# Kernel tuning notes

Measured on AMD Instinct MI355X. Metric: run time of the kernel, lower is better.

## Reference

```python
import jax, jax.numpy as jnp
import numpy as np


def setup_inputs() -> dict:
    key = jax.random.key(0)
    kq, kk, kv = jax.random.split(key, 3)
    S, D = 8192, 128
    return {
        "Q": jax.random.normal(kq, (S, D), dtype=jnp.float32),
        "K": jax.random.normal(kk, (S, D), dtype=jnp.float32),
        "V": jax.random.normal(kv, (S, D), dtype=jnp.float32),
    }


def reference(Q, K, V):
    d_k = Q.shape[-1]
    scale = 1.0 / jnp.sqrt(jnp.asarray(d_k, Q.dtype))
    scores = (Q @ K.T) * scale          # [S, S]
    attn = jax.nn.softmax(scores, axis=-1)
    return attn @ V                     # [S, Dv]
```

## Files before the change

kernel.cpp:

```cpp
#include <hip/hip_runtime.h>
#include <hip/hip_bf16.h>
#include <hip/hip_fp16.h>
#include <math.h>

typedef __attribute__((ext_vector_type(8))) short short8;
typedef __attribute__((ext_vector_type(16))) float f32x16;
typedef __attribute__((ext_vector_type(4))) unsigned short ushort4v;
typedef __attribute__((ext_vector_type(4))) unsigned int uint4v;

#define S 8192
#define D 128
#define QBLK 128
#define KVB 32

__device__ __forceinline__ unsigned short f2bf(float f) {
    unsigned int x = __float_as_uint(f);
    unsigned int r = x + 0x7fffu + ((x >> 16) & 1u);
    return (unsigned short)(r >> 16);
}

__device__ __forceinline__ unsigned int cvtpk(float a, float b) {
    unsigned int r;
    asm("v_cvt_pk_bf16_f32 %0, %1, %2" : "=v"(r) : "v"(a), "v"(b));
    return r;
}

__device__ __forceinline__ float fexp2(float x) { return __builtin_amdgcn_exp2f(x); }

__device__ __forceinline__ void gl_lds16(const unsigned short* g, unsigned short* l) {
    __builtin_amdgcn_global_load_lds(
        (const __attribute__((address_space(1))) unsigned int*)g,
        (__attribute__((address_space(3))) unsigned int*)l, 16, 0, 0);
}

__device__ __forceinline__ void plswap(unsigned int& a, unsigned int& b, int hi) {
#if __has_builtin(__builtin_amdgcn_permlane32_swap)
    auto r = __builtin_amdgcn_permlane32_swap((int)a, (int)b, false, false);
    a = (unsigned int)r[0];
    b = (unsigned int)r[1];
#else
    unsigned int xa = (unsigned int)__shfl_xor((int)a, 32, 64);
    unsigned int xb = (unsigned int)__shfl_xor((int)b, 32, 64);
    unsigned int na = hi ? xb : a;
    unsigned int nb = hi ? b : xa;
    a = na; b = nb;
#endif
}

union W4 { unsigned int u[4]; short8 v; };

__global__ __launch_bounds__(256) void prep_kv(const float* __restrict__ K,
                                               const float* __restrict__ V,
                                               unsigned short* __restrict__ Kb,
                                               unsigned short* __restrict__ Vt) {
    __shared__ unsigned short T[64][72];
    const float scale = 0.12751743022854459f;
    int s0 = blockIdx.x * 64, d0 = blockIdx.y * 64;
    int tr = threadIdx.x >> 4, tc = (threadIdx.x & 15) * 4;
#pragma unroll
    for (int p = 0; p < 4; ++p) {
        int r = p * 16 + tr;
        float4 kf = *reinterpret_cast<const float4*>(K + (size_t)(s0 + r) * D + d0 + tc);
        ushort4v ko = { f2bf(kf.x * scale), f2bf(kf.y * scale),
                        f2bf(kf.z * scale), f2bf(kf.w * scale) };
        *reinterpret_cast<ushort4v*>(Kb + (size_t)(s0 + r) * D + d0 + tc) = ko;
        float4 v = *reinterpret_cast<const float4*>(V + (size_t)(s0 + r) * D + d0 + tc);
        ushort4v vo = { f2bf(v.x), f2bf(v.y), f2bf(v.z), f2bf(v.w) };
        *reinterpret_cast<ushort4v*>(&T[r][tc]) = vo;
    }
    __syncthreads();
#pragma unroll
    for (int p = 0; p < 4; ++p) {
        int dr = p * 16 + tr;
        ushort4v o = { T[tc + 0][dr], T[tc + 1][dr], T[tc + 2][dr], T[tc + 3][dr] };
        *reinterpret_cast<ushort4v*>(Vt + (size_t)(d0 + dr) * S + s0 + tc) = o;
    }
}

#define QKOP(acc, kc) (acc) = __builtin_amdgcn_mfma_f32_32x32x16_bf16(              \
    *reinterpret_cast<const short8*>(                                               \
        &Kl[(size_t)c31 * 128 + (((2 * (kc) + hi) ^ (c31 & 15)) * 8)]),             \
    qf[kc], (acc), 0, 0, 0)

#define PVOP(oo, pp, dt, off) (oo) = __builtin_amdgcn_mfma_f32_32x32x16_bf16(       \
    (pp).v,                                                                          \
    *reinterpret_cast<const short8*>(                                               \
        &Vl[((dt) * 32 + c31) * 32 + ((((off) + hi) ^ sw) * 8)]),                    \
    (oo), 0, 0, 0)

#define SMEX(PD0, PD1)                                                               \
    {                                                                                \
        float e[16];                                                                 \
        _Pragma("unroll")                                                            \
        for (int i = 0; i < 16; ++i) e[i] = fexp2(sa[i] + sb[i]);                    \
        float t0 = (e[0] + e[1]) + (e[2] + e[3]);                                    \
        float t1 = (e[4] + e[5]) + (e[6] + e[7]);                                    \
        float t2 = (e[8] + e[9]) + (e[10] + e[11]);                                  \
        float t3 = (e[12] + e[13]) + (e[14] + e[15]);                                \
        l_r += (t0 + t1) + (t2 + t3);                                                \
        unsigned int wd[8];                                                          \
        _Pragma("unroll")                                                            \
        for (int u = 0; u < 8; ++u) wd[u] = cvtpk(e[2 * u], e[2 * u + 1]);           \
        plswap(wd[0], wd[2], hi); plswap(wd[1], wd[3], hi);                          \
        plswap(wd[4], wd[6], hi); plswap(wd[5], wd[7], hi);                          \
        PD0.u[0] = wd[0]; PD0.u[1] = wd[1]; PD0.u[2] = wd[2]; PD0.u[3] = wd[3];      \
        PD1.u[0] = wd[4]; PD1.u[1] = wd[5]; PD1.u[2] = wd[6]; PD1.u[3] = wd[7];      \
    }

#define STAGE_K(RING) do {                                                           \
    gl_lds16(kg[0], &Klds[RING][(w * 2 + 0) * 512]); kg[0] += (size_t)KVB * D;       \
    gl_lds16(kg[1], &Klds[RING][(w * 2 + 1) * 512]); kg[1] += (size_t)KVB * D;       \
} while (0)

#define STAGE_V(RING) do {                                                           \
    gl_lds16(vg[0], &Vlds[RING][(w * 2 + 0) * 512]); vg[0] += KVB;                   \
    gl_lds16(vg[1], &Vlds[RING][(w * 2 + 1) * 512]); vg[1] += KVB;                   \
} while (0)

#define PHASE_BARRIER() do {                                                         \
    asm volatile("s_waitcnt vmcnt(0)" ::: "memory");                                 \
    __builtin_amdgcn_s_barrier();                                                    \
    __builtin_amdgcn_sched_barrier(0);                                               \
} while (0)

#define SUBTILE(KR, VR, PP0, PP1, QQ0, QQ1)                                          \
    {                                                                                \
        const unsigned short* Kl = Klds[KR];                                         \
        const unsigned short* Vl = Vlds[VR];                                         \
        f32x16 sa, sb;                                                               \
        _Pragma("unroll")                                                            \
        for (int i = 0; i < 16; ++i) { sa[i] = 0.f; sb[i] = 0.f; }                   \
        __builtin_amdgcn_s_setprio(1);                                               \
        QKOP(sa, 0); QKOP(sb, 1);                                                    \
        PVOP(o0, PP0, 0, 0); QKOP(sa, 2); PVOP(o0, PP1, 0, 2);                       \
        QKOP(sb, 3); PVOP(o1, PP0, 1, 0); QKOP(sa, 4); PVOP(o1, PP1, 1, 2);          \
        QKOP(sb, 5); PVOP(o2, PP0, 2, 0); QKOP(sa, 6); PVOP(o2, PP1, 2, 2);          \
        QKOP(sb, 7); PVOP(o3, PP0, 3, 0); PVOP(o3, PP1, 3, 2);                       \
        __builtin_amdgcn_s_setprio(0);                                               \
        SMEX(QQ0, QQ1);                                                              \
    }

#define SUBTILE_NOPV(KR, QQ0, QQ1)                                                   \
    {                                                                                \
        const unsigned short* Kl = Klds[KR];                                         \
        f32x16 sa, sb;                                                               \
        _Pragma("unroll")                                                            \
        for (int i = 0; i < 16; ++i) { sa[i] = 0.f; sb[i] = 0.f; }                   \
        __builtin_amdgcn_s_setprio(1);                                               \
        QKOP(sa, 0); QKOP(sb, 1); QKOP(sa, 2); QKOP(sb, 3);                          \
        QKOP(sa, 4); QKOP(sb, 5); QKOP(sa, 6); QKOP(sb, 7);                          \
        __builtin_amdgcn_s_setprio(0);                                               \
        SMEX(QQ0, QQ1);                                                              \
    }

#define ATTN_SETUP()                                                                 \
    const int tid  = threadIdx.x;                                                    \
    const int w    = tid >> 6;                                                       \
    const int lane = tid & 63;                                                       \
    const int hi   = lane >> 5;                                                      \
    const int c31  = lane & 31;                                                      \
    const int sw   = (c31 >> 1) & 3;                                                 \
    const int bid  = blockIdx.x;                                                     \
    const int sp   = bid % split;                                                    \
    const int qb   = bid / split;                                                    \
    const int chunk  = S / split;                                                    \
    const int kv0    = sp * chunk;                                                   \
    const int ntiles = chunk / KVB;                                                  \
    short8 qf[8];                                                                    \
    {                                                                                \
        const float* qrow = Q + (size_t)(qb * QBLK + w * 32 + c31) * D;              \
        _Pragma("unroll")                                                            \
        for (int kc = 0; kc < 8; ++kc) {                                             \
            float4 x = *reinterpret_cast<const float4*>(qrow + kc * 16 + hi * 8);    \
            float4 y = *reinterpret_cast<const float4*>(qrow + kc * 16 + hi * 8 + 4);\
            W4 u;                                                                    \
            u.u[0] = cvtpk(x.x, x.y); u.u[1] = cvtpk(x.z, x.w);                      \
            u.u[2] = cvtpk(y.x, y.y); u.u[3] = cvtpk(y.z, y.w);                      \
            qf[kc] = u.v;                                                            \
        }                                                                            \
    }                                                                                \
    const unsigned short* kg[2];                                                     \
    const unsigned short* vg[2];                                                     \
    _Pragma("unroll")                                                                \
    for (int i = 0; i < 2; ++i) {                                                    \
        int krow = w * 8 + i * 4 + (lane >> 4);                                      \
        int kch  = (lane & 15) ^ (krow & 15);                                        \
        kg[i] = Kb + (size_t)(kv0 + krow) * D + kch * 8;                             \
        int vrow = w * 32 + i * 16 + (lane >> 2);                                    \
        int vch  = (lane & 3) ^ ((vrow >> 1) & 3);                                   \
        vg[i] = Vtg + (size_t)vrow * S + kv0 + vch * 8;                              \
    }                                                                                \
    f32x16 o0, o1, o2, o3;                                                           \
    _Pragma("unroll")                                                                \
    for (int i = 0; i < 16; ++i) { o0[i] = 0.f; o1[i] = 0.f; o2[i] = 0.f; o3[i] = 0.f; } \
    float l_r = 0.f;                                                                 \
    W4 pX0, pX1, pY0, pY1;

#define ATTN_EPILOGUE()                                                              \
    float l_tot = l_r + __shfl_xor(l_r, 32, 64);                                     \
    if (split == 1) {                                                                \
        _Pragma("unroll")                                                            \
        for (int reg = 0; reg < 16; ++reg) {                                         \
            int crow = (reg & 3) + 8 * (reg >> 2) + 4 * hi;                          \
            float lr  = __shfl(l_tot, crow, 64);                                     \
            float inv = 1.f / lr;                                                    \
            size_t rb = (size_t)(qb * QBLK + w * 32 + crow) * D;                     \
            out[rb +  0 + c31] = o0[reg] * inv;                                      \
            out[rb + 32 + c31] = o1[reg] * inv;                                      \
            out[rb + 64 + c31] = o2[reg] * inv;                                      \
            out[rb + 96 + c31] = o3[reg] * inv;                                      \
        }                                                                            \
    } else {                                                                         \
        __half* Opart = wsO + (size_t)(qb * split + sp) * (QBLK * D);                \
        _Pragma("unroll")                                                            \
        for (int reg = 0; reg < 16; ++reg) {                                         \
            int crow = (reg & 3) + 8 * (reg >> 2) + 4 * hi;                          \
            size_t rb = (size_t)(w * 32 + crow) * D;                                 \
            Opart[rb +  0 + c31] = __float2half(o0[reg]);                            \
            Opart[rb + 32 + c31] = __float2half(o1[reg]);                            \
            Opart[rb + 64 + c31] = __float2half(o2[reg]);                            \
            Opart[rb + 96 + c31] = __float2half(o3[reg]);                            \
        }                                                                            \
        if (hi == 0)                                                                 \
            wsL[(size_t)(qb * split + sp) * QBLK + w * 32 + c31] = l_tot;            \
    }

__global__ __launch_bounds__(256, 2) void attn_fwd_d4(
    const float* __restrict__ Q, const unsigned short* __restrict__ Kb,
    const unsigned short* __restrict__ Vtg, float* __restrict__ out,
    __half* __restrict__ wsO, float* __restrict__ wsL, int split)
{
    __shared__ __attribute__((aligned(16))) unsigned short Klds[4][KVB * D];
    __shared__ __attribute__((aligned(16))) unsigned short Vlds[4][D * KVB];

    ATTN_SETUP();

    STAGE_K(0); STAGE_K(1); STAGE_V(0);

    PHASE_BARRIER();
    STAGE_K(2); STAGE_K(3);
    STAGE_V(1); STAGE_V(2);
    SUBTILE_NOPV(0, pY0, pY1);
    SUBTILE(1, 0, pY0, pY1, pX0, pX1);

    const int npair = ntiles / 4 - 1;
#pragma unroll 1
    for (int j = 0; j < npair; ++j) {
        PHASE_BARRIER();
        STAGE_K(0); STAGE_K(1);
        STAGE_V(3); STAGE_V(0);
        SUBTILE(2, 1, pX0, pX1, pY0, pY1);
        SUBTILE(3, 2, pY0, pY1, pX0, pX1);
        PHASE_BARRIER();
        STAGE_K(2); STAGE_K(3);
        STAGE_V(1); STAGE_V(2);
        SUBTILE(0, 3, pX0, pX1, pY0, pY1);
        SUBTILE(1, 0, pY0, pY1, pX0, pX1);
    }

    PHASE_BARRIER();
    STAGE_V(3);
    SUBTILE(2, 1, pX0, pX1, pY0, pY1);
    SUBTILE(3, 2, pY0, pY1, pX0, pX1);

    PHASE_BARRIER();
    {
        const unsigned short* Vl = Vlds[3];
        __builtin_amdgcn_s_setprio(1);
        PVOP(o0, pX0, 0, 0); PVOP(o0, pX1, 0, 2);
        PVOP(o1, pX0, 1, 0); PVOP(o1, pX1, 1, 2);
        PVOP(o2, pX0, 2, 0); PVOP(o2, pX1, 2, 2);
        PVOP(o3, pX0, 3, 0); PVOP(o3, pX1, 3, 2);
        __builtin_amdgcn_s_setprio(0);
    }

    ATTN_EPILOGUE();
}

__global__ __launch_bounds__(256, 2) void attn_fwd_d2(
    const float* __restrict__ Q, const unsigned short* __restrict__ Kb,
    const unsigned short* __restrict__ Vtg, float* __restrict__ out,
    __half* __restrict__ wsO, float* __restrict__ wsL, int split)
{
    __shared__ __attribute__((aligned(16))) unsigned short Klds[2][KVB * D];
    __shared__ __attribute__((aligned(16))) unsigned short Vlds[2][D * KVB];

    ATTN_SETUP();

    STAGE_K(0);
    PHASE_BARRIER();

    STAGE_K(1); STAGE_V(0);
    SUBTILE_NOPV(0, pY0, pY1);

    const int npair = ntiles / 2 - 1;
#pragma unroll 1
    for (int j = 0; j < npair; ++j) {
        PHASE_BARRIER();
        STAGE_K(0); STAGE_V(1);
        SUBTILE(1, 0, pY0, pY1, pX0, pX1);
        PHASE_BARRIER();
        STAGE_K(1); STAGE_V(0);
        SUBTILE(0, 1, pX0, pX1, pY0, pY1);
    }

    PHASE_BARRIER();
    STAGE_V(1);
    SUBTILE(1, 0, pY0, pY1, pX0, pX1);

    PHASE_BARRIER();
    {
        const unsigned short* Vl = Vlds[1];
        __builtin_amdgcn_s_setprio(1);
        PVOP(o0, pX0, 0, 0); PVOP(o0, pX1, 0, 2);
        PVOP(o1, pX0, 1, 0); PVOP(o1, pX1, 1, 2);
        PVOP(o2, pX0, 2, 0); PVOP(o2, pX1, 2, 2);
        PVOP(o3, pX0, 3, 0); PVOP(o3, pX1, 3, 2);
        __builtin_amdgcn_s_setprio(0);
    }

    ATTN_EPILOGUE();
}

__global__ void attn_combine(const __half* __restrict__ wsO,
                             const float* __restrict__ wsL,
                             float* __restrict__ out, int split)
{
    int idx = blockIdx.x * blockDim.x + threadIdx.x;
    if (idx >= S * D / 8) return;
    int row = idx >> 4;
    int g   = (idx & 15) * 8;
    int qb = row >> 7, rloc = row & 127;
    float acc[8];
#pragma unroll
    for (int i = 0; i < 8; ++i) acc[i] = 0.f;
    float L = 0.f;
    for (int s = 0; s < split; ++s) {
        size_t b = (size_t)(qb * split + s);
        const __half* p = wsO + b * (QBLK * D) + (size_t)rloc * D + g;
        uint4v u = *reinterpret_cast<const uint4v*>(p);
#pragma unroll
        for (int i = 0; i < 4; ++i) {
            unsigned int wbits = u[i];
            __half2 h = *reinterpret_cast<__half2*>(&wbits);
            float2 f = __half22float2(h);
            acc[2 * i]     += f.x;
            acc[2 * i + 1] += f.y;
        }
        L += wsL[b * QBLK + rloc];
    }
    float inv = 1.f / L;
    size_t ob = (size_t)row * D + g;
    float4 w0 = { acc[0] * inv, acc[1] * inv, acc[2] * inv, acc[3] * inv };
    float4 w1 = { acc[4] * inv, acc[5] * inv, acc[6] * inv, acc[7] * inv };
    *reinterpret_cast<float4*>(out + ob)     = w0;
    *reinterpret_cast<float4*>(out + ob + 4) = w1;
}

extern "C" void kernel_launch(void* const* d_in, const int* in_sizes, int n_in,
                              void* d_out, int out_size, void* d_ws, size_t ws_size,
                              hipStream_t stream) {
    const float* Q = (const float*)d_in[0];
    const float* K = (const float*)d_in[1];
    const float* V = (const float*)d_in[2];
    float* out = (float*)d_out;

    size_t base = 2ull * S * D * sizeof(unsigned short);
    size_t need16 = base + 16ull * S * D * sizeof(__half) + 16ull * S * sizeof(float);
    int split;
    if (ws_size >= need16) {
        split = 16;
    } else {
        split = 1;
        for (int sp = 8; sp >= 2; sp >>= 1) {
            size_t need = base + (size_t)sp * S * D * sizeof(__half)
                        + (size_t)sp * S * sizeof(float);
            if (ws_size >= need) { split = sp; break; }
        }
    }

    unsigned short* Kb = (unsigned short*)d_ws;
    unsigned short* Vt = Kb + (size_t)S * D;
    __half* wsO = (__half*)(Vt + (size_t)S * D);
    float* wsL = (float*)(wsO + (size_t)split * S * D);

    prep_kv<<<dim3(S / 64, D / 64), 256, 0, stream>>>(K, V, Kb, Vt);
    if (split == 16)
        attn_fwd_d2<<<(S / QBLK) * split, 256, 0, stream>>>(Q, Kb, Vt, out, wsO, wsL, split);
    else
        attn_fwd_d4<<<(S / QBLK) * split, 256, 0, stream>>>(Q, Kb, Vt, out, wsO, wsL, split);
    if (split > 1)
        attn_combine<<<(S * D / 8 + 255) / 256, 256, 0, stream>>>(wsO, wsL, out, split);
}
```

Measured before the change: 65.76 us.

## Load K fragments directly from global into registers, drop K LDS staging

Adds a new attention kernel that streams K tiles straight from global memory into per-wave register fragments, double-buffered and prefetched during softmax, while V still goes through a 4-deep LDS ring. The split selection drops the split-16 path and caps the split at 8, launching this kernel for every split. This removes LDS traffic and barrier work for K, at the cost of higher register pressure (launch bounds lowered to one block per SIMD set) and redundant global K reads across the four waves.

```diff
diff --git a/kernel.cpp b/kernel.cpp
--- a/kernel.cpp
+++ b/kernel.cpp
@@ -82,11 +82,21 @@
         &Kl[(size_t)c31 * 128 + (((2 * (kc) + hi) ^ (c31 & 15)) * 8)]),             \
     qf[kc], (acc), 0, 0, 0)
 
+#define QKOPR(acc, kc, KR) (acc) = __builtin_amdgcn_mfma_f32_32x32x16_bf16(         \
+    KR[kc], qf[kc], (acc), 0, 0, 0)
+
 #define PVOP(oo, pp, dt, off) (oo) = __builtin_amdgcn_mfma_f32_32x32x16_bf16(       \
     (pp).v,                                                                          \
     *reinterpret_cast<const short8*>(                                               \
         &Vl[((dt) * 32 + c31) * 32 + ((((off) + hi) ^ sw) * 8)]),                    \
     (oo), 0, 0, 0)
+
+#define LOADK(KR, GP) do {                                                           \
+    _Pragma("unroll")                                                                \
+    for (int kc_ = 0; kc_ < 8; ++kc_)                                                \
+        KR[kc_] = *reinterpret_cast<const short8*>((GP) + kc_ * 16);                 \
+    (GP) += 2 * KVB * D;                                                             \
+} while (0)
 
 #define SMEX(PD0, PD1)                                                               \
     {                                                                                \
@@ -150,6 +160,36 @@
         QKOP(sa, 0); QKOP(sb, 1); QKOP(sa, 2); QKOP(sb, 3);                          \
         QKOP(sa, 4); QKOP(sb, 5); QKOP(sa, 6); QKOP(sb, 7);                          \
         __builtin_amdgcn_s_setprio(0);                                               \
+        SMEX(QQ0, QQ1);                                                              \
+    }
+
+#define SUBTILE_KG(VR, PP0, PP1, QQ0, QQ1, KR, PRELOAD)                              \
+    {                                                                                \
+        const unsigned short* Vl = Vlds[VR];                                         \
+        f32x16 sa, sb;                                                               \
+        _Pragma("unroll")                                                            \
+        for (int i = 0; i < 16; ++i) { sa[i] = 0.f; sb[i] = 0.f; }                   \
+        __builtin_amdgcn_s_setprio(1);                                               \
+        QKOPR(sa, 0, KR); QKOPR(sb, 1, KR);                                          \
+        PVOP(o0, PP0, 0, 0); QKOPR(sa, 2, KR); PVOP(o0, PP1, 0, 2);                  \
+        QKOPR(sb, 3, KR); PVOP(o1, PP0, 1, 0); QKOPR(sa, 4, KR); PVOP(o1, PP1, 1, 2);\
+        QKOPR(sb, 5, KR); PVOP(o2, PP0, 2, 0); QKOPR(sa, 6, KR); PVOP(o2, PP1, 2, 2);\
+        QKOPR(sb, 7, KR); PVOP(o3, PP0, 3, 0); PVOP(o3, PP1, 3, 2);                  \
+        __builtin_amdgcn_s_setprio(0);                                               \
+        PRELOAD;                                                                     \
+        SMEX(QQ0, QQ1);                                                              \
+    }
+
+#define SUBTILE_NOPV_KG(QQ0, QQ1, KR, PRELOAD)                                       \
+    {                                                                                \
+        f32x16 sa, sb;                                                               \
+        _Pragma("unroll")                                                            \
+        for (int i = 0; i < 16; ++i) { sa[i] = 0.f; sb[i] = 0.f; }                   \
+        __builtin_amdgcn_s_setprio(1);                                               \
+        QKOPR(sa, 0, KR); QKOPR(sb, 1, KR); QKOPR(sa, 2, KR); QKOPR(sb, 3, KR);      \
+        QKOPR(sa, 4, KR); QKOPR(sb, 5, KR); QKOPR(sa, 6, KR); QKOPR(sb, 7, KR);      \
+        __builtin_amdgcn_s_setprio(0);                                               \
+        PRELOAD;                                                                     \
         SMEX(QQ0, QQ1);                                                              \
     }
 
@@ -179,13 +219,9 @@
             qf[kc] = u.v;                                                            \
         }                                                                            \
     }                                                                                \
-    const unsigned short* kg[2];                                                     \
     const unsigned short* vg[2];                                                     \
     _Pragma("unroll")                                                                \
     for (int i = 0; i < 2; ++i) {                                                    \
-        int krow = w * 8 + i * 4 + (lane >> 4);                                      \
-        int kch  = (lane & 15) ^ (krow & 15);                                        \
-        kg[i] = Kb + (size_t)(kv0 + krow) * D + kch * 8;                             \
         int vrow = w * 32 + i * 16 + (lane >> 2);                                    \
         int vch  = (lane & 3) ^ ((vrow >> 1) & 3);                                   \
         vg[i] = Vtg + (size_t)vrow * S + kv0 + vch * 8;                              \
@@ -225,6 +261,60 @@
             wsL[(size_t)(qb * split + sp) * QBLK + w * 32 + c31] = l_tot;            \
     }
 
+__global__ __launch_bounds__(256, 1) void attn_fwd_kg(
+    const float* __restrict__ Q, const unsigned short* __restrict__ Kb,
+    const unsigned short* __restrict__ Vtg, float* __restrict__ out,
+    __half* __restrict__ wsO, float* __restrict__ wsL, int split)
+{
+    __shared__ __attribute__((aligned(16))) unsigned short Vlds[4][D * KVB];
+
+    ATTN_SETUP();
+
+    const unsigned short* kgA = Kb + ((size_t)(kv0 + c31) * D + hi * 8);
+    const unsigned short* kgB = kgA + (size_t)KVB * D;
+    short8 krA[8], krB[8];
+
+    LOADK(krA, kgA);
+    LOADK(krB, kgB);
+    STAGE_V(0);
+
+    PHASE_BARRIER();
+    STAGE_V(1); STAGE_V(2);
+    SUBTILE_NOPV_KG(pY0, pY1, krA, LOADK(krA, kgA));
+    SUBTILE_KG(0, pY0, pY1, pX0, pX1, krB, LOADK(krB, kgB));
+
+    const int npair = ntiles / 4 - 1;
+#pragma unroll 1
+    for (int j = 0; j < npair; ++j) {
+        PHASE_BARRIER();
+        STAGE_V(3); STAGE_V(0);
+        SUBTILE_KG(1, pX0, pX1, pY0, pY1, krA, LOADK(krA, kgA));
+        SUBTILE_KG(2, pY0, pY1, pX0, pX1, krB, LOADK(krB, kgB));
+        PHASE_BARRIER();
+        STAGE_V(1); STAGE_V(2);
+        SUBTILE_KG(3, pX0, pX1, pY0, pY1, krA, LOADK(krA, kgA));
+        SUBTILE_KG(0, pY0, pY1, pX0, pX1, krB, LOADK(krB, kgB));
+    }
+
+    PHASE_BARRIER();
+    STAGE_V(3);
+    SUBTILE_KG(1, pX0, pX1, pY0, pY1, krA, ((void)0));
+    SUBTILE_KG(2, pY0, pY1, pX0, pX1, krB, ((void)0));
+
+    PHASE_BARRIER();
+    {
+        const unsigned short* Vl = Vlds[3];
+        __builtin_amdgcn_s_setprio(1);
+        PVOP(o0, pX0, 0, 0); PVOP(o0, pX1, 0, 2);
+        PVOP(o1, pX0, 1, 0); PVOP(o1, pX1, 1, 2);
+        PVOP(o2, pX0, 2, 0); PVOP(o2, pX1, 2, 2);
+        PVOP(o3, pX0, 3, 0); PVOP(o3, pX1, 3, 2);
+        __builtin_amdgcn_s_setprio(0);
+    }
+
+    ATTN_EPILOGUE();
+}
+
 __global__ __launch_bounds__(256, 2) void attn_fwd_d4(
     const float* __restrict__ Q, const unsigned short* __restrict__ Kb,
     const unsigned short* __restrict__ Vtg, float* __restrict__ out,
@@ -234,6 +324,13 @@
     __shared__ __attribute__((aligned(16))) unsigned short Vlds[4][D * KVB];
 
     ATTN_SETUP();
+    const unsigned short* kg[2];
+#pragma unroll
+    for (int i = 0; i < 2; ++i) {
+        int krow = w * 8 + i * 4 + (lane >> 4);
+        int kch  = (lane & 15) ^ (krow & 15);
+        kg[i] = Kb + (size_t)(kv0 + krow) * D + kch * 8;
+    }
 
     STAGE_K(0); STAGE_K(1); STAGE_V(0);
 
@@ -266,51 +363,6 @@
     PHASE_BARRIER();
     {
         const unsigned short* Vl = Vlds[3];
-        __builtin_amdgcn_s_setprio(1);
-        PVOP(o0, pX0, 0, 0); PVOP(o0, pX1, 0, 2);
-        PVOP(o1, pX0, 1, 0); PVOP(o1, pX1, 1, 2);
-        PVOP(o2, pX0, 2, 0); PVOP(o2, pX1, 2, 2);
-        PVOP(o3, pX0, 3, 0); PVOP(o3, pX1, 3, 2);
-        __builtin_amdgcn_s_setprio(0);
-    }
-
-    ATTN_EPILOGUE();
-}
-
-__global__ __launch_bounds__(256, 2) void attn_fwd_d2(
-    const float* __restrict__ Q, const unsigned short* __restrict__ Kb,
-    const unsigned short* __restrict__ Vtg, float* __restrict__ out,
-    __half* __restrict__ wsO, float* __restrict__ wsL, int split)
-{
-    __shared__ __attribute__((aligned(16))) unsigned short Klds[2][KVB * D];
-    __shared__ __attribute__((aligned(16))) unsigned short Vlds[2][D * KVB];
-
-    ATTN_SETUP();
-
-    STAGE_K(0);
-    PHASE_BARRIER();
-
-    STAGE_K(1); STAGE_V(0);
-    SUBTILE_NOPV(0, pY0, pY1);
-
-    const int npair = ntiles / 2 - 1;
-#pragma unroll 1
-    for (int j = 0; j < npair; ++j) {
-        PHASE_BARRIER();
-        STAGE_K(0); STAGE_V(1);
-        SUBTILE(1, 0, pY0, pY1, pX0, pX1);
-        PHASE_BARRIER();
-        STAGE_K(1); STAGE_V(0);
-        SUBTILE(0, 1, pX0, pX1, pY0, pY1);
-    }
-
-    PHASE_BARRIER();
-    STAGE_V(1);
-    SUBTILE(1, 0, pY0, pY1, pX0, pX1);
-
-    PHASE_BARRIER();
-    {
-        const unsigned short* Vl = Vlds[1];
         __builtin_amdgcn_s_setprio(1);
         PVOP(o0, pX0, 0, 0); PVOP(o0, pX1, 0, 2);
         PVOP(o1, pX0, 1, 0); PVOP(o1, pX1, 1, 2);
@@ -366,17 +418,11 @@
     float* out = (float*)d_out;
 
     size_t base = 2ull * S * D * sizeof(unsigned short);
-    size_t need16 = base + 16ull * S * D * sizeof(__half) + 16ull * S * sizeof(float);
-    int split;
-    if (ws_size >= need16) {
-        split = 16;
-    } else {
-        split = 1;
-        for (int sp = 8; sp >= 2; sp >>= 1) {
-            size_t need = base + (size_t)sp * S * D * sizeof(__half)
-                        + (size_t)sp * S * sizeof(float);
-            if (ws_size >= need) { split = sp; break; }
-        }
+    int split = 1;
+    for (int sp = 8; sp >= 2; sp >>= 1) {
+        size_t need = base + (size_t)sp * S * D * sizeof(__half)
+                    + (size_t)sp * S * sizeof(float);
+        if (ws_size >= need) { split = sp; break; }
     }
 
     unsigned short* Kb = (unsigned short*)d_ws;
@@ -385,10 +431,7 @@
     float* wsL = (float*)(wsO + (size_t)split * S * D);
 
     prep_kv<<<dim3(S / 64, D / 64), 256, 0, stream>>>(K, V, Kb, Vt);
-    if (split == 16)
-        attn_fwd_d2<<<(S / QBLK) * split, 256, 0, stream>>>(Q, Kb, Vt, out, wsO, wsL, split);
-    else
-        attn_fwd_d4<<<(S / QBLK) * split, 256, 0, stream>>>(Q, Kb, Vt, out, wsO, wsL, split);
+    attn_fwd_kg<<<(S / QBLK) * split, 256, 0, stream>>>(Q, Kb, Vt, out, wsO, wsL, split);
     if (split > 1)
         attn_combine<<<(S * D / 8 + 255) / 256, 256, 0, stream>>>(wsO, wsL, out, split);
 }
```

Result: slower. 103.3 us (+57.0%).
